# Kernel optimization log

Hardware: AMD Instinct MI355X
Metric: run time of the kernel (lower is better)

Reference implementation:

```python
import jax, jax.numpy as jnp
import numpy as np

N_QUBITS = 6
N_LAYERS = 3
B, D_IN, HID, D_OUT = 131072, 32, 16, 1


def _apply_1q(state, gate, q):
    """Apply a 1-qubit gate. state: [B,2,...,2] (qubit q at axis q+1).
    gate: [2,2] (shared) or [B,2,2] (per-sample)."""
    s = jnp.moveaxis(state, q + 1, 1)
    if gate.ndim == 2:
        s = jnp.einsum('ij,bj...->bi...', gate, s)
    else:
        s = jnp.einsum('bij,bj...->bi...', gate, s)
    return jnp.moveaxis(s, 1, q + 1)


def _cnot(state, c, t):
    """CNOT with control c, target t (static wire indices)."""
    idx = (slice(None),) * (c + 1) + (1,)
    sub = state[idx]                      # control axis dropped
    ta = t + 1 if t < c else t            # target axis inside sub
    return state.at[idx].set(jnp.flip(sub, axis=ta))


def _expvals_z(state, n):
    p = state.real ** 2 + state.imag ** 2  # probabilities [B,2,...,2]
    outs = []
    for q in range(n):
        axes = tuple(a for a in range(1, n + 1) if a != q + 1)
        m = p.sum(axes)                    # [B,2]
        outs.append(m[:, 0] - m[:, 1])
    return jnp.stack(outs, axis=-1)        # [B,n]


def quantum_circuit(angles, weights):
    """AngleEmbedding(RY) + BasicEntanglerLayers(RX + CNOT ring), PauliZ expvals."""
    b = angles.shape[0]
    state = jnp.zeros((b,) + (2,) * N_QUBITS, jnp.complex64)
    state = state.at[(slice(None),) + (0,) * N_QUBITS].set(1.0 + 0.0j)
    # per-sample RY embedding
    half = angles * 0.5
    c, s = jnp.cos(half), jnp.sin(half)
    for q in range(N_QUBITS):
        g = jnp.stack([jnp.stack([c[:, q], -s[:, q]], -1),
                       jnp.stack([s[:, q],  c[:, q]], -1)], -2).astype(jnp.complex64)
        state = _apply_1q(state, g, q)
    # entangler layers: RX(w) on each wire, then CNOT ring
    for l in range(N_LAYERS):
        hw = weights[l] * 0.5
        cw = jnp.cos(hw).astype(jnp.complex64)
        sw = (-1j) * jnp.sin(hw).astype(jnp.complex64)
        for q in range(N_QUBITS):
            g = jnp.stack([jnp.stack([cw[q], sw[q]]),
                           jnp.stack([sw[q], cw[q]])])
            state = _apply_1q(state, g, q)
        for q in range(N_QUBITS):
            state = _cnot(state, q, (q + 1) % N_QUBITS)
    return _expvals_z(state, N_QUBITS)


def setup_inputs() -> dict:
    key = jax.random.key(0)
    ks = jax.random.split(key, 11)
    def lin_w(k, fi, fo):
        bnd = 1.0 / np.sqrt(fi)
        return jax.random.uniform(k, (fi, fo), jnp.float32, -bnd, bnd)
    def lin_b(k, fi, fo):
        bnd = 1.0 / np.sqrt(fi)
        return jax.random.uniform(k, (fo,), jnp.float32, -bnd, bnd)
    return {
        'features': jax.random.normal(ks[0], (B, D_IN), jnp.float32),
        'baseline': jax.random.normal(ks[1], (B, D_OUT), jnp.float32),
        'enc_w1': lin_w(ks[2], D_IN, HID), 'enc_b1': lin_b(ks[3], D_IN, HID),
        'enc_w2': lin_w(ks[4], HID, N_QUBITS), 'enc_b2': lin_b(ks[5], HID, N_QUBITS),
        'q_weights': jax.random.uniform(ks[6], (N_LAYERS, N_QUBITS), jnp.float32, 0.0, 2.0 * np.pi),
        'head_w1': lin_w(ks[7], N_QUBITS, HID), 'head_b1': lin_b(ks[8], N_QUBITS, HID),
        'head_w2': lin_w(ks[9], HID, D_OUT), 'head_b2': lin_b(ks[10], HID, D_OUT),
    }


def reference(features, baseline, enc_w1, enc_b1, enc_w2, enc_b2, q_weights,
              head_w1, head_b1, head_w2, head_b2):
    h = jax.nn.gelu(features @ enc_w1 + enc_b1, approximate=False)
    angles = jnp.tanh(h @ enc_w2 + enc_b2)              # [B, n_qubits]
    q_feats = quantum_circuit(angles, q_weights)         # [B, n_qubits]
    r = jax.nn.gelu(q_feats @ head_w1 + head_b1, approximate=False) @ head_w2 + head_b2
    return baseline + r
```

## Files before the change

kernel.cpp:

```cpp
#include <hip/hip_runtime.h>
#include <math.h>


typedef float f32x2 __attribute__((ext_vector_type(2)));

__host__ __device__ constexpr int Lmap(int j) {
    int b5=(j>>5)&1, b4=(j>>4)&1, b3=(j>>3)&1, b2=(j>>2)&1, b1=(j>>1)&1, b0=j&1;
    int o5=b5^b4, o4=b4^b3, o3=b3^b2, o2=b2^b1, o1=b1^b0, o0=b0^b5^b4;
    return (o5<<5)|(o4<<4)|(o3<<3)|(o2<<2)|(o1<<1)|o0;
}
__host__ __device__ constexpr int Linv(int j) {
    int o5=(j>>5)&1, o4=(j>>4)&1, o3=(j>>3)&1, o2=(j>>2)&1, o1=(j>>1)&1, o0=j&1;
    int b4 = o5^o4^o3^o2^o1^o0;
    int b5 = b4^o5;
    int b3 = b4^o4;
    int b2 = b3^o3;
    int b1 = b2^o2;
    int b0 = b1^o1;
    return (b5<<5)|(b4<<4)|(b3<<3)|(b2<<2)|(b1<<1)|b0;
}
__host__ __device__ constexpr int MPc(int q) {
    int m = 1 << (5 - q);
    m = Linv(m); m = Linv(m); m = Linv(m);
    return m;
}
__host__ __device__ constexpr int popc6(int m) {
    int c = 0;
    for (int p = 0; p < 6; ++p) c += (m >> p) & 1;
    return c;
}

__device__ __forceinline__ float fast_rcp(float x) { return __builtin_amdgcn_rcpf(x); }

__device__ __forceinline__ float fast_tanh(float x) {
    float e = __expf(2.0f * x);
    return fmaf(-2.0f, fast_rcp(1.0f + e), 1.0f);
}
__device__ __forceinline__ float fast_gelu(float x) {
    float x3 = x * x * x;
    float t  = fast_tanh(fmaf(0.044715f, x3, x) * 0.7978845608028654f);
    return 0.5f * x * (1.0f + t);
}

template<int Q>
__device__ __forceinline__ float zq_eval(const float (&u2)[6][2], const float (&u01)[6],
                                         const float (&K)[48]) {
    constexpr int mp = MPc(Q);
    constexpr int F  = (~mp) & 63;
    constexpr int nf = 6 - popc6(mp);
    float cq = 1.0f;
    #pragma unroll
    for (int p = 0; p < 6; ++p) if ((mp >> p) & 1) cq *= u01[p];
    float acc = 0.0f;
    #pragma unroll
    for (int r = 0; r < (1 << nf); ++r) {
        float t = K[Q * 8 + r];
        int k = nf;
        #pragma unroll
        for (int p = 5; p >= 0; --p) if ((F >> p) & 1) { --k; t *= u2[p][(r >> k) & 1]; }
        acc += t;
    }
    return acc * cq;
}

__global__ __launch_bounds__(256) __attribute__((amdgpu_waves_per_eu(2, 2)))
void qrr_kernel(const float* __restrict__ features,
                const float* __restrict__ baseline,
                const float* __restrict__ enc_w1,
                const float* __restrict__ enc_b1,
                const float* __restrict__ enc_w2,
                const float* __restrict__ enc_b2,
                const float* __restrict__ q_weights,
                const float* __restrict__ head_w1,
                const float* __restrict__ head_b1,
                const float* __restrict__ head_w2,
                const float* __restrict__ head_b2,
                float* __restrict__ out,
                int n)
{
    __shared__ float phi[64];
    __shared__ __align__(16) float KTs[48];
    const int tid = threadIdx.x;

    if (tid < 64) {
        int jl = tid;
        float acc = 0.0f;
        for (int l = 0; l < 3; ++l) {
            for (int q = 0; q < 6; ++q)
                acc += q_weights[l * 6 + q] * (((jl >> (5 - q)) & 1) ? 0.5f : -0.5f);
            jl = Lmap(jl);
        }
        phi[tid] = acc;
    }
    __syncthreads();

    if (tid < 48) {
        const int q = tid >> 3, r = tid & 7;
        const int mp = Linv(Linv(Linv(1 << (5 - q))));
        const int F  = (~mp) & 63;
        const int nf = __popc(F), pm = 6 - nf;
        float kv = 0.0f;
        if (r < (1 << nf)) {
            int jb = 0, k = nf;
            for (int p = 5; p >= 0; --p)
                if ((F >> p) & 1) { --k; if ((r >> k) & 1) jb |= 1 << p; }
            float s = 0.0f;
            for (int e = 0; e < (1 << pm); ++e) {
                int je = 0, kk = pm;
                for (int p = 5; p >= 0; --p)
                    if ((mp >> p) & 1) { --kk; if ((e >> kk) & 1) je |= 1 << p; }
                const int j0 = jb | je;
                s += __cosf(phi[j0 ^ mp] - phi[j0]);
            }
            kv = s * (1.0f / 64.0f);
        }
        KTs[tid] = kv;
    }
    __syncthreads();

    float K[48];
    {
        const float4* kp = reinterpret_cast<const float4*>(KTs);
        #pragma unroll
        for (int i = 0; i < 12; ++i) {
            float4 v = kp[i];
            K[4*i+0] = v.x; K[4*i+1] = v.y; K[4*i+2] = v.z; K[4*i+3] = v.w;
        }
    }

    const int b = blockIdx.x * 256 + tid;
    if (b >= n) return;

    float f[32];
    {
        const float4* fp = reinterpret_cast<const float4*>(features + (size_t)b * 32);
        #pragma unroll
        for (int k = 0; k < 8; ++k) {
            float4 v = fp[k];
            f[4*k+0] = v.x; f[4*k+1] = v.y; f[4*k+2] = v.z; f[4*k+3] = v.w;
        }
    }
    const float base = baseline[b];

    f32x2 h2[8];
    {
        const f32x2* bb = reinterpret_cast<const f32x2*>(enc_b1);
        #pragma unroll
        for (int o = 0; o < 8; ++o) h2[o] = bb[o];
    }
    #pragma unroll
    for (int i = 0; i < 32; ++i) {
        const f32x2 fv = {f[i], f[i]};
        const f32x2* w = reinterpret_cast<const f32x2*>(enc_w1 + i * 16);
        #pragma unroll
        for (int o = 0; o < 8; ++o)
            h2[o] = __builtin_elementwise_fma(fv, w[o], h2[o]);
    }
    float h[16];
    #pragma unroll
    for (int o = 0; o < 8; ++o) {
        h[2*o]   = fast_gelu(h2[o].x);
        h[2*o+1] = fast_gelu(h2[o].y);
    }

    float u2[6][2], u01[6];
    #pragma unroll
    for (int q = 0; q < 6; ++q) {
        float a = enc_b2[q];
        #pragma unroll
        for (int i = 0; i < 16; ++i)
            a = fmaf(h[i], enc_w2[i * 6 + q], a);
        const float w = fast_tanh(a);
        float sn, cs;
        __sincosf(w, &sn, &cs);
        const int p = 5 - q;
        u2[p][0] = 1.0f + sn;
        u2[p][1] = 1.0f - sn;
        u01[p]   = cs;
    }

    float z[6];
    z[0] = zq_eval<0>(u2, u01, K);
    z[1] = zq_eval<1>(u2, u01, K);
    z[2] = zq_eval<2>(u2, u01, K);
    z[3] = zq_eval<3>(u2, u01, K);
    z[4] = zq_eval<4>(u2, u01, K);
    z[5] = zq_eval<5>(u2, u01, K);

    f32x2 hh2[8];
    {
        const f32x2* bb = reinterpret_cast<const f32x2*>(head_b1);
        #pragma unroll
        for (int o = 0; o < 8; ++o) hh2[o] = bb[o];
    }
    #pragma unroll
    for (int i = 0; i < 6; ++i) {
        const f32x2 zv = {z[i], z[i]};
        const f32x2* w = reinterpret_cast<const f32x2*>(head_w1 + i * 16);
        #pragma unroll
        for (int o = 0; o < 8; ++o)
            hh2[o] = __builtin_elementwise_fma(zv, w[o], hh2[o]);
    }
    float r = head_b2[0];
    #pragma unroll
    for (int o = 0; o < 8; ++o) {
        r = fmaf(fast_gelu(hh2[o].x), head_w2[2*o],     r);
        r = fmaf(fast_gelu(hh2[o].y), head_w2[2*o + 1], r);
    }

    out[b] = base + r;
}

extern "C" void kernel_launch(void* const* d_in, const int* in_sizes, int n_in,
                              void* d_out, int out_size, void* d_ws, size_t ws_size,
                              hipStream_t stream) {
    const float* features = (const float*)d_in[0];
    const float* baseline = (const float*)d_in[1];
    const float* enc_w1   = (const float*)d_in[2];
    const float* enc_b1   = (const float*)d_in[3];
    const float* enc_w2   = (const float*)d_in[4];
    const float* enc_b2   = (const float*)d_in[5];
    const float* q_weights= (const float*)d_in[6];
    const float* head_w1  = (const float*)d_in[7];
    const float* head_b1  = (const float*)d_in[8];
    const float* head_w2  = (const float*)d_in[9];
    const float* head_b2  = (const float*)d_in[10];
    float* out = (float*)d_out;

    const int n = in_sizes[0] / 32;
    const int block = 256;
    const int grid = (n + block - 1) / block;
    qrr_kernel<<<grid, block, 0, stream>>>(features, baseline,
                                           enc_w1, enc_b1, enc_w2, enc_b2,
                                           q_weights,
                                           head_w1, head_b1, head_w2, head_b2,
                                           out, n);
}
```

Measured before the change: 15.53 us.

## Process two samples per thread with packed f32x2 math across the whole pipeline

Each thread now handles two samples (b and b+n/2) packed into f32x2 lanes, so the encoder MLP, quantum expectation evaluation and head MLP run as packed FMAs over sample pairs instead of pairing output neurons. The grid halves, so the per-block phi/K setup is amortised over twice as many samples. Occupancy hints are relaxed to waves_per_eu(1,2) to leave room for the larger register footprint. Odd n would drop the last sample, and higher register pressure may reduce latency hiding.

```diff
diff --git a/kernel.cpp b/kernel.cpp
--- a/kernel.cpp
+++ b/kernel.cpp
@@ -32,29 +32,34 @@
 
 __device__ __forceinline__ float fast_rcp(float x) { return __builtin_amdgcn_rcpf(x); }
 
-__device__ __forceinline__ float fast_tanh(float x) {
-    float e = __expf(2.0f * x);
-    return fmaf(-2.0f, fast_rcp(1.0f + e), 1.0f);
-}
-__device__ __forceinline__ float fast_gelu(float x) {
-    float x3 = x * x * x;
-    float t  = fast_tanh(fmaf(0.044715f, x3, x) * 0.7978845608028654f);
-    return 0.5f * x * (1.0f + t);
+__device__ __forceinline__ f32x2 bc2(float s) { return (f32x2){s, s}; }
+
+__device__ __forceinline__ f32x2 fast_tanh2(f32x2 x) {
+    float eA = __expf(2.0f * x.x);
+    float eB = __expf(2.0f * x.y);
+    return (f32x2){ fmaf(-2.0f, fast_rcp(1.0f + eA), 1.0f),
+                    fmaf(-2.0f, fast_rcp(1.0f + eB), 1.0f) };
+}
+__device__ __forceinline__ f32x2 fast_gelu2(f32x2 x) {
+    f32x2 x2 = x * x;
+    f32x2 inner = x * __builtin_elementwise_fma(x2, bc2(0.0356774081f), bc2(0.7978845608f));
+    f32x2 t = fast_tanh2(inner);
+    return bc2(0.5f) * x * (bc2(1.0f) + t);
 }
 
 template<int Q>
-__device__ __forceinline__ float zq_eval(const float (&u2)[6][2], const float (&u01)[6],
-                                         const float (&K)[48]) {
+__device__ __forceinline__ f32x2 zq_eval2(const f32x2 (&u2)[6][2], const f32x2 (&u01)[6],
+                                          const float (&K)[48]) {
     constexpr int mp = MPc(Q);
     constexpr int F  = (~mp) & 63;
     constexpr int nf = 6 - popc6(mp);
-    float cq = 1.0f;
+    f32x2 cq = bc2(1.0f);
     #pragma unroll
     for (int p = 0; p < 6; ++p) if ((mp >> p) & 1) cq *= u01[p];
-    float acc = 0.0f;
+    f32x2 acc = bc2(0.0f);
     #pragma unroll
     for (int r = 0; r < (1 << nf); ++r) {
-        float t = K[Q * 8 + r];
+        f32x2 t = bc2(K[Q * 8 + r]);
         int k = nf;
         #pragma unroll
         for (int p = 5; p >= 0; --p) if ((F >> p) & 1) { --k; t *= u2[p][(r >> k) & 1]; }
@@ -63,7 +68,7 @@
     return acc * cq;
 }
 
-__global__ __launch_bounds__(256) __attribute__((amdgpu_waves_per_eu(2, 2)))
+__global__ __launch_bounds__(256) __attribute__((amdgpu_waves_per_eu(1, 2)))
 void qrr_kernel(const float* __restrict__ features,
                 const float* __restrict__ baseline,
                 const float* __restrict__ enc_w1,
@@ -76,7 +81,7 @@
                 const float* __restrict__ head_w2,
                 const float* __restrict__ head_b2,
                 float* __restrict__ out,
-                int n)
+                int half_n)
 {
     __shared__ float phi[64];
     __shared__ __align__(16) float KTs[48];
@@ -118,6 +123,55 @@
     }
     __syncthreads();
 
+    const int t = blockIdx.x * 256 + tid;
+    if (t >= half_n) return;
+    const int bA = t, bB = t + half_n;
+
+    f32x2 f2[32];
+    {
+        const float4* fa = reinterpret_cast<const float4*>(features + (size_t)bA * 32);
+        const float4* fb = reinterpret_cast<const float4*>(features + (size_t)bB * 32);
+        #pragma unroll
+        for (int k = 0; k < 8; ++k) {
+            float4 va = fa[k];
+            float4 vb = fb[k];
+            f2[4*k+0] = (f32x2){va.x, vb.x};
+            f2[4*k+1] = (f32x2){va.y, vb.y};
+            f2[4*k+2] = (f32x2){va.z, vb.z};
+            f2[4*k+3] = (f32x2){va.w, vb.w};
+        }
+    }
+    const float baseA = baseline[bA];
+    const float baseB = baseline[bB];
+
+    f32x2 h2[16];
+    #pragma unroll
+    for (int o = 0; o < 16; ++o) h2[o] = bc2(enc_b1[o]);
+    #pragma unroll
+    for (int i = 0; i < 32; ++i) {
+        #pragma unroll
+        for (int o = 0; o < 16; ++o)
+            h2[o] = __builtin_elementwise_fma(f2[i], bc2(enc_w1[i * 16 + o]), h2[o]);
+    }
+    #pragma unroll
+    for (int o = 0; o < 16; ++o) h2[o] = fast_gelu2(h2[o]);
+
+    f32x2 u2[6][2], u01[6];
+    #pragma unroll
+    for (int q = 0; q < 6; ++q) {
+        f32x2 a = bc2(enc_b2[q]);
+        #pragma unroll
+        for (int i = 0; i < 16; ++i)
+            a = __builtin_elementwise_fma(h2[i], bc2(enc_w2[i * 6 + q]), a);
+        f32x2 w = fast_tanh2(a);
+        f32x2 sn = { __sinf(w.x), __sinf(w.y) };
+        f32x2 cs = { __cosf(w.x), __cosf(w.y) };
+        const int p = 5 - q;
+        u2[p][0] = bc2(1.0f) + sn;
+        u2[p][1] = bc2(1.0f) - sn;
+        u01[p]   = cs;
+    }
+
     float K[48];
     {
         const float4* kp = reinterpret_cast<const float4*>(KTs);
@@ -128,87 +182,30 @@
         }
     }
 
-    const int b = blockIdx.x * 256 + tid;
-    if (b >= n) return;
-
-    float f[32];
-    {
-        const float4* fp = reinterpret_cast<const float4*>(features + (size_t)b * 32);
-        #pragma unroll
-        for (int k = 0; k < 8; ++k) {
-            float4 v = fp[k];
-            f[4*k+0] = v.x; f[4*k+1] = v.y; f[4*k+2] = v.z; f[4*k+3] = v.w;
-        }
-    }
-    const float base = baseline[b];
-
-    f32x2 h2[8];
-    {
-        const f32x2* bb = reinterpret_cast<const f32x2*>(enc_b1);
-        #pragma unroll
-        for (int o = 0; o < 8; ++o) h2[o] = bb[o];
-    }
-    #pragma unroll
-    for (int i = 0; i < 32; ++i) {
-        const f32x2 fv = {f[i], f[i]};
-        const f32x2* w = reinterpret_cast<const f32x2*>(enc_w1 + i * 16);
-        #pragma unroll
-        for (int o = 0; o < 8; ++o)
-            h2[o] = __builtin_elementwise_fma(fv, w[o], h2[o]);
-    }
-    float h[16];
-    #pragma unroll
-    for (int o = 0; o < 8; ++o) {
-        h[2*o]   = fast_gelu(h2[o].x);
-        h[2*o+1] = fast_gelu(h2[o].y);
-    }
-
-    float u2[6][2], u01[6];
-    #pragma unroll
-    for (int q = 0; q < 6; ++q) {
-        float a = enc_b2[q];
-        #pragma unroll
-        for (int i = 0; i < 16; ++i)
-            a = fmaf(h[i], enc_w2[i * 6 + q], a);
-        const float w = fast_tanh(a);
-        float sn, cs;
-        __sincosf(w, &sn, &cs);
-        const int p = 5 - q;
-        u2[p][0] = 1.0f + sn;
-        u2[p][1] = 1.0f - sn;
-        u01[p]   = cs;
-    }
-
-    float z[6];
-    z[0] = zq_eval<0>(u2, u01, K);
-    z[1] = zq_eval<1>(u2, u01, K);
-    z[2] = zq_eval<2>(u2, u01, K);
-    z[3] = zq_eval<3>(u2, u01, K);
-    z[4] = zq_eval<4>(u2, u01, K);
-    z[5] = zq_eval<5>(u2, u01, K);
-
-    f32x2 hh2[8];
-    {
-        const f32x2* bb = reinterpret_cast<const f32x2*>(head_b1);
-        #pragma unroll
-        for (int o = 0; o < 8; ++o) hh2[o] = bb[o];
-    }
+    f32x2 z[6];
+    z[0] = zq_eval2<0>(u2, u01, K);
+    z[1] = zq_eval2<1>(u2, u01, K);
+    z[2] = zq_eval2<2>(u2, u01, K);
+    z[3] = zq_eval2<3>(u2, u01, K);
+    z[4] = zq_eval2<4>(u2, u01, K);
+    z[5] = zq_eval2<5>(u2, u01, K);
+
+    f32x2 hh2[16];
+    #pragma unroll
+    for (int o = 0; o < 16; ++o) hh2[o] = bc2(head_b1[o]);
     #pragma unroll
     for (int i = 0; i < 6; ++i) {
-        const f32x2 zv = {z[i], z[i]};
-        const f32x2* w = reinterpret_cast<const f32x2*>(head_w1 + i * 16);
-        #pragma unroll
-        for (int o = 0; o < 8; ++o)
-            hh2[o] = __builtin_elementwise_fma(zv, w[o], hh2[o]);
-    }
-    float r = head_b2[0];
-    #pragma unroll
-    for (int o = 0; o < 8; ++o) {
-        r = fmaf(fast_gelu(hh2[o].x), head_w2[2*o],     r);
-        r = fmaf(fast_gelu(hh2[o].y), head_w2[2*o + 1], r);
-    }
-
-    out[b] = base + r;
+        #pragma unroll
+        for (int o = 0; o < 16; ++o)
+            hh2[o] = __builtin_elementwise_fma(z[i], bc2(head_w1[i * 16 + o]), hh2[o]);
+    }
+    f32x2 r2 = bc2(head_b2[0]);
+    #pragma unroll
+    for (int o = 0; o < 16; ++o)
+        r2 = __builtin_elementwise_fma(fast_gelu2(hh2[o]), bc2(head_w2[o]), r2);
+
+    out[bA] = baseA + r2.x;
+    out[bB] = baseB + r2.y;
 }
 
 extern "C" void kernel_launch(void* const* d_in, const int* in_sizes, int n_in,
@@ -228,11 +225,12 @@
     float* out = (float*)d_out;
 
     const int n = in_sizes[0] / 32;
+    const int half_n = n >> 1;
     const int block = 256;
-    const int grid = (n + block - 1) / block;
+    const int grid = (half_n + block - 1) / block;
     qrr_kernel<<<grid, block, 0, stream>>>(features, baseline,
                                            enc_w1, enc_b1, enc_w2, enc_b2,
                                            q_weights,
                                            head_w1, head_b1, head_w2, head_b2,
-                                           out, n);
-}
+                                           out, half_n);
+}
```

After: 17.40 us. 1.12x slower.

## Split each sample across two wavefronts with LDS exchange between stages

Applied to the files above, without the earlier changes.

Each sample is now processed by two threads in different wavefronts. Each thread handles half of the encoder input features, half of the hidden units, three of the qubit expectations and half of the head, and partial results are exchanged through shared memory with block barriers. The aim is to halve per-thread register pressure and serial work so more waves fit per EU (the waves_per_eu hint is raised from 2 to 4), giving more parallelism for latency hiding. The cost is doubled thread count, several extra __syncthreads and LDS traffic, and the tail-bounds check is dropped because n is assumed divisible by 128. GELU's polynomial is also refactored to save one multiply.

```diff
diff --git a/kernel.cpp b/kernel.cpp
--- a/kernel.cpp
+++ b/kernel.cpp
@@ -31,20 +31,25 @@
 }
 
 __device__ __forceinline__ float fast_rcp(float x) { return __builtin_amdgcn_rcpf(x); }
+__device__ __forceinline__ f32x2 bc2(float s) { return (f32x2){s, s}; }
 
 __device__ __forceinline__ float fast_tanh(float x) {
     float e = __expf(2.0f * x);
     return fmaf(-2.0f, fast_rcp(1.0f + e), 1.0f);
 }
 __device__ __forceinline__ float fast_gelu(float x) {
-    float x3 = x * x * x;
-    float t  = fast_tanh(fmaf(0.044715f, x3, x) * 0.7978845608028654f);
+    float x2 = x * x;
+    float inner = x * fmaf(x2, 0.0356774081f, 0.7978845608f);
+    float t = fast_tanh(inner);
     return 0.5f * x * (1.0f + t);
+}
+__device__ __forceinline__ f32x2 fast_gelu2(f32x2 x) {
+    return (f32x2){ fast_gelu(x.x), fast_gelu(x.y) };
 }
 
 template<int Q>
 __device__ __forceinline__ float zq_eval(const float (&u2)[6][2], const float (&u01)[6],
-                                         const float (&K)[48]) {
+                                         const float (&K)[24]) {
     constexpr int mp = MPc(Q);
     constexpr int F  = (~mp) & 63;
     constexpr int nf = 6 - popc6(mp);
@@ -54,7 +59,7 @@
     float acc = 0.0f;
     #pragma unroll
     for (int r = 0; r < (1 << nf); ++r) {
-        float t = K[Q * 8 + r];
+        float t = K[(Q % 3) * 8 + r];
         int k = nf;
         #pragma unroll
         for (int p = 5; p >= 0; --p) if ((F >> p) & 1) { --k; t *= u2[p][(r >> k) & 1]; }
@@ -63,7 +68,7 @@
     return acc * cq;
 }
 
-__global__ __launch_bounds__(256) __attribute__((amdgpu_waves_per_eu(2, 2)))
+__global__ __launch_bounds__(256) __attribute__((amdgpu_waves_per_eu(4, 4)))
 void qrr_kernel(const float* __restrict__ features,
                 const float* __restrict__ baseline,
                 const float* __restrict__ enc_w1,
@@ -80,7 +85,16 @@
 {
     __shared__ float phi[64];
     __shared__ __align__(16) float KTs[48];
-    const int tid = threadIdx.x;
+    __shared__ __align__(16) f32x2 XH[2][2][4][64];
+    __shared__ float XP[2][2][3][64];
+    __shared__ float XU[2][2][9][64];
+    __shared__ float XZ[2][2][3][64];
+    __shared__ float XR[2][64];
+
+    const int tid  = threadIdx.x;
+    const int lane = tid & 63;
+    const int subw = (tid >> 6) & 1;
+    const int P    = tid >> 7;
 
     if (tid < 64) {
         int jl = tid;
@@ -116,99 +130,171 @@
         }
         KTs[tid] = kv;
     }
-    __syncthreads();
-
-    float K[48];
+
+    const int s = blockIdx.x * 128 + P * 64 + lane;
+
+    float f[16];
     {
-        const float4* kp = reinterpret_cast<const float4*>(KTs);
-        #pragma unroll
-        for (int i = 0; i < 12; ++i) {
+        const float4* fp = reinterpret_cast<const float4*>(
+            features + (size_t)s * 32 + subw * 16);
+        #pragma unroll
+        for (int k = 0; k < 4; ++k) {
+            float4 v = fp[k];
+            f[4*k+0] = v.x; f[4*k+1] = v.y; f[4*k+2] = v.z; f[4*k+3] = v.w;
+        }
+    }
+    float base = 0.0f;
+    if (subw == 0) base = baseline[s];
+
+    const float* w1p = enc_w1 + subw * 256;
+    f32x2 part2[8];
+    #pragma unroll
+    for (int o = 0; o < 8; ++o) part2[o] = bc2(0.0f);
+    #pragma unroll
+    for (int i = 0; i < 16; ++i) {
+        const f32x2 fv = bc2(f[i]);
+        const f32x2* w = reinterpret_cast<const f32x2*>(w1p + i * 16);
+        #pragma unroll
+        for (int o = 0; o < 8; ++o)
+            part2[o] = __builtin_elementwise_fma(fv, w[o], part2[o]);
+    }
+    if (subw == 0) {
+        #pragma unroll
+        for (int k = 0; k < 4; ++k) XH[P][0][k][lane] = part2[4 + k];
+    } else {
+        #pragma unroll
+        for (int k = 0; k < 4; ++k) XH[P][1][k][lane] = part2[k];
+    }
+    __syncthreads();
+
+    f32x2 g2[4];
+    {
+        const f32x2* b1p = reinterpret_cast<const f32x2*>(enc_b1 + subw * 8);
+        if (subw == 0) {
+            #pragma unroll
+            for (int k = 0; k < 4; ++k)
+                g2[k] = fast_gelu2(part2[k] + XH[P][1][k][lane] + b1p[k]);
+        } else {
+            #pragma unroll
+            for (int k = 0; k < 4; ++k)
+                g2[k] = fast_gelu2(part2[4 + k] + XH[P][0][k][lane] + b1p[k]);
+        }
+    }
+    float g[8];
+    #pragma unroll
+    for (int k = 0; k < 4; ++k) { g[2*k] = g2[k].x; g[2*k+1] = g2[k].y; }
+
+    const float* w2p = enc_w2 + (subw * 8) * 6;
+    float pq[6] = {0,0,0,0,0,0};
+    #pragma unroll
+    for (int k = 0; k < 8; ++k) {
+        #pragma unroll
+        for (int q = 0; q < 6; ++q)
+            pq[q] = fmaf(g[k], w2p[k * 6 + q], pq[q]);
+    }
+    if (subw == 0) {
+        #pragma unroll
+        for (int j = 0; j < 3; ++j) XP[P][0][j][lane] = pq[3 + j];
+    } else {
+        #pragma unroll
+        for (int j = 0; j < 3; ++j) XP[P][1][j][lane] = pq[j];
+    }
+    __syncthreads();
+
+    float u20[3], u21[3], u01m[3];
+    {
+        #pragma unroll
+        for (int j = 0; j < 3; ++j) {
+            float a;
+            if (subw == 0) a = pq[j]     + XP[P][1][j][lane] + enc_b2[j];
+            else           a = pq[3 + j] + XP[P][0][j][lane] + enc_b2[3 + j];
+            const float w = fast_tanh(a);
+            const float sn = __sinf(w), cs = __cosf(w);
+            u20[j] = 1.0f + sn;
+            u21[j] = 1.0f - sn;
+            u01m[j] = cs;
+        }
+    }
+    #pragma unroll
+    for (int j = 0; j < 3; ++j) {
+        XU[P][subw][j][lane]     = u20[j];
+        XU[P][subw][3 + j][lane] = u21[j];
+        XU[P][subw][6 + j][lane] = u01m[j];
+    }
+    __syncthreads();
+
+    float u2[6][2], u01[6];
+    if (subw == 0) {
+        u2[5][0]=u20[0]; u2[5][1]=u21[0]; u01[5]=u01m[0];
+        u2[4][0]=u20[1]; u2[4][1]=u21[1]; u01[4]=u01m[1];
+        u2[3][0]=u20[2]; u2[3][1]=u21[2]; u01[3]=u01m[2];
+        u2[2][0]=XU[P][1][0][lane]; u2[2][1]=XU[P][1][3][lane]; u01[2]=XU[P][1][6][lane];
+        u2[1][0]=XU[P][1][1][lane]; u2[1][1]=XU[P][1][4][lane]; u01[1]=XU[P][1][7][lane];
+        u2[0][0]=XU[P][1][2][lane]; u2[0][1]=XU[P][1][5][lane]; u01[0]=XU[P][1][8][lane];
+    } else {
+        u2[2][0]=u20[0]; u2[2][1]=u21[0]; u01[2]=u01m[0];
+        u2[1][0]=u20[1]; u2[1][1]=u21[1]; u01[1]=u01m[1];
+        u2[0][0]=u20[2]; u2[0][1]=u21[2]; u01[0]=u01m[2];
+        u2[5][0]=XU[P][0][0][lane]; u2[5][1]=XU[P][0][3][lane]; u01[5]=XU[P][0][6][lane];
+        u2[4][0]=XU[P][0][1][lane]; u2[4][1]=XU[P][0][4][lane]; u01[4]=XU[P][0][7][lane];
+        u2[3][0]=XU[P][0][2][lane]; u2[3][1]=XU[P][0][5][lane]; u01[3]=XU[P][0][8][lane];
+    }
+
+    float K[24];
+    {
+        const float4* kp = reinterpret_cast<const float4*>(&KTs[subw * 24]);
+        #pragma unroll
+        for (int i = 0; i < 6; ++i) {
             float4 v = kp[i];
             K[4*i+0] = v.x; K[4*i+1] = v.y; K[4*i+2] = v.z; K[4*i+3] = v.w;
         }
     }
 
-    const int b = blockIdx.x * 256 + tid;
-    if (b >= n) return;
-
-    float f[32];
-    {
-        const float4* fp = reinterpret_cast<const float4*>(features + (size_t)b * 32);
-        #pragma unroll
-        for (int k = 0; k < 8; ++k) {
-            float4 v = fp[k];
-            f[4*k+0] = v.x; f[4*k+1] = v.y; f[4*k+2] = v.z; f[4*k+3] = v.w;
-        }
-    }
-    const float base = baseline[b];
-
-    f32x2 h2[8];
-    {
-        const f32x2* bb = reinterpret_cast<const f32x2*>(enc_b1);
-        #pragma unroll
-        for (int o = 0; o < 8; ++o) h2[o] = bb[o];
-    }
-    #pragma unroll
-    for (int i = 0; i < 32; ++i) {
-        const f32x2 fv = {f[i], f[i]};
-        const f32x2* w = reinterpret_cast<const f32x2*>(enc_w1 + i * 16);
-        #pragma unroll
-        for (int o = 0; o < 8; ++o)
-            h2[o] = __builtin_elementwise_fma(fv, w[o], h2[o]);
-    }
-    float h[16];
-    #pragma unroll
-    for (int o = 0; o < 8; ++o) {
-        h[2*o]   = fast_gelu(h2[o].x);
-        h[2*o+1] = fast_gelu(h2[o].y);
-    }
-
-    float u2[6][2], u01[6];
-    #pragma unroll
-    for (int q = 0; q < 6; ++q) {
-        float a = enc_b2[q];
-        #pragma unroll
-        for (int i = 0; i < 16; ++i)
-            a = fmaf(h[i], enc_w2[i * 6 + q], a);
-        const float w = fast_tanh(a);
-        float sn, cs;
-        __sincosf(w, &sn, &cs);
-        const int p = 5 - q;
-        u2[p][0] = 1.0f + sn;
-        u2[p][1] = 1.0f - sn;
-        u01[p]   = cs;
-    }
+    float zm[3];
+    if (subw == 0) {
+        zm[0] = zq_eval<0>(u2, u01, K);
+        zm[1] = zq_eval<1>(u2, u01, K);
+        zm[2] = zq_eval<2>(u2, u01, K);
+    } else {
+        zm[0] = zq_eval<3>(u2, u01, K);
+        zm[1] = zq_eval<4>(u2, u01, K);
+        zm[2] = zq_eval<5>(u2, u01, K);
+    }
+    #pragma unroll
+    for (int j = 0; j < 3; ++j) XZ[P][subw][j][lane] = zm[j];
+    __syncthreads();
 
     float z[6];
-    z[0] = zq_eval<0>(u2, u01, K);
-    z[1] = zq_eval<1>(u2, u01, K);
-    z[2] = zq_eval<2>(u2, u01, K);
-    z[3] = zq_eval<3>(u2, u01, K);
-    z[4] = zq_eval<4>(u2, u01, K);
-    z[5] = zq_eval<5>(u2, u01, K);
-
-    f32x2 hh2[8];
-    {
-        const f32x2* bb = reinterpret_cast<const f32x2*>(head_b1);
-        #pragma unroll
-        for (int o = 0; o < 8; ++o) hh2[o] = bb[o];
-    }
+    if (subw == 0) {
+        z[0]=zm[0]; z[1]=zm[1]; z[2]=zm[2];
+        z[3]=XZ[P][1][0][lane]; z[4]=XZ[P][1][1][lane]; z[5]=XZ[P][1][2][lane];
+    } else {
+        z[3]=zm[0]; z[4]=zm[1]; z[5]=zm[2];
+        z[0]=XZ[P][0][0][lane]; z[1]=XZ[P][0][1][lane]; z[2]=XZ[P][0][2][lane];
+    }
+
+    const float* hw1p = head_w1 + subw * 8;
+    const float* hb1p = head_b1 + subw * 8;
+    const float* hw2p = head_w2 + subw * 8;
+    float hh[8];
+    #pragma unroll
+    for (int k = 0; k < 8; ++k) hh[k] = hb1p[k];
     #pragma unroll
     for (int i = 0; i < 6; ++i) {
-        const f32x2 zv = {z[i], z[i]};
-        const f32x2* w = reinterpret_cast<const f32x2*>(head_w1 + i * 16);
-        #pragma unroll
-        for (int o = 0; o < 8; ++o)
-            hh2[o] = __builtin_elementwise_fma(zv, w[o], hh2[o]);
-    }
-    float r = head_b2[0];
-    #pragma unroll
-    for (int o = 0; o < 8; ++o) {
-        r = fmaf(fast_gelu(hh2[o].x), head_w2[2*o],     r);
-        r = fmaf(fast_gelu(hh2[o].y), head_w2[2*o + 1], r);
-    }
-
-    out[b] = base + r;
+        const float zi = z[i];
+        #pragma unroll
+        for (int k = 0; k < 8; ++k)
+            hh[k] = fmaf(zi, hw1p[i * 16 + k], hh[k]);
+    }
+    float rp = 0.0f;
+    #pragma unroll
+    for (int k = 0; k < 8; ++k)
+        rp = fmaf(fast_gelu(hh[k]), hw2p[k], rp);
+
+    if (subw == 1) XR[P][lane] = rp;
+    __syncthreads();
+    if (subw == 0)
+        out[s] = base + rp + XR[P][lane] + head_b2[0];
 }
 
 extern "C" void kernel_launch(void* const* d_in, const int* in_sizes, int n_in,
@@ -228,11 +314,10 @@
     float* out = (float*)d_out;
 
     const int n = in_sizes[0] / 32;
-    const int block = 256;
-    const int grid = (n + block - 1) / block;
-    qrr_kernel<<<grid, block, 0, stream>>>(features, baseline,
-                                           enc_w1, enc_b1, enc_w2, enc_b2,
-                                           q_weights,
-                                           head_w1, head_b1, head_w2, head_b2,
-                                           out, n);
-}
+    const int grid = n / 128;
+    qrr_kernel<<<grid, 256, 0, stream>>>(features, baseline,
+                                         enc_w1, enc_b1, enc_w2, enc_b2,
+                                         q_weights,
+                                         head_w1, head_b1, head_w2, head_b2,
+                                         out, n);
+}
```

Measured after the change: 20.88 us. +34.4%, slower.
